# Optimization experiments

Measured on AMD Instinct MI355X. Metric: run time of the kernel, lower is better.

## Reference

```python
import jax, jax.numpy as jnp
import numpy as np

B = 2        # batch size
G = 128      # dense grid extent per axis
N = 200000   # occupied voxels
M = 200000   # query points
C = 128      # feature dim
IGNORE = -1  # ignore_label

# 8 trilinear corner offsets [8,3]
_OFFSETS = jnp.array([[i, j, k] for i in (0, 1) for j in (0, 1) for k in (0, 1)], dtype=jnp.int32)


def setup_inputs() -> dict:
    key = jax.random.key(0)
    k1, k2, k3, k4, k5 = jax.random.split(key, 5)
    xyz = jax.random.randint(k1, (N, 3), 0, G).astype(jnp.int32)
    bids = jnp.sort(jax.random.randint(k2, (N,), 0, B)).astype(jnp.int32)  # sorted batch ids (sparse tensor layout)
    coords = jnp.concatenate([bids[:, None], xyz], axis=1)                 # [N,4]
    features_3d = jax.random.normal(k3, (N, C), dtype=jnp.float32)
    qxyz = jax.random.uniform(k4, (M, 3), minval=0.0, maxval=float(G - 1))
    qb = jnp.sort(jax.random.randint(k5, (M,), 0, B)).astype(jnp.float32)
    query_points = jnp.concatenate([qb[:, None], qxyz], axis=1)            # [M,4]
    return {"features_3d": features_3d, "coords": coords, "query_points": query_points}


def _trilinear(features_3d, coords, query_points):
    bids = coords[:, 0]
    # per-batch coordinate shift (torch.amin per batch)
    shift = jax.ops.segment_min(coords[:, 1:], bids, num_segments=B)       # [B,3]
    c = coords[:, 1:] - shift[bids]                                        # [N,3]
    qb = query_points[:, 0].astype(jnp.int32)                              # [M]
    q = query_points[:, 1:] - shift[qb].astype(query_points.dtype)         # [M,3]

    # dense occupancy grid: voxel row index, IGNORE where empty
    occ = jnp.full((B, G, G, G), IGNORE, dtype=jnp.int32)
    occ = occ.at[bids, c[:, 0], c[:, 1], c[:, 2]].set(jnp.arange(N, dtype=jnp.int32))

    base = jnp.floor(q).astype(jnp.int32)                                  # [M,3]
    frac = q - base.astype(q.dtype)                                        # [M,3]
    corner = base[:, None, :] + _OFFSETS[None]                             # [M,8,3]
    # trilinear weights: prod over dims of frac (offset=1) or 1-frac (offset=0)
    w = jnp.prod(jnp.where(_OFFSETS[None] == 1, frac[:, None, :], 1.0 - frac[:, None, :]), axis=-1)  # [M,8]

    in_bounds = jnp.all((corner >= 0) & (corner < G), axis=-1)             # [M,8]
    cc = jnp.clip(corner, 0, G - 1)
    idx = occ[qb[:, None], cc[..., 0], cc[..., 1], cc[..., 2]]             # [M,8]
    valid = in_bounds & (idx != IGNORE)

    interp_idx = jnp.where(valid, idx, IGNORE)                             # [M,8]
    interp_w = jnp.where(valid, w, 0.0).astype(features_3d.dtype)          # [M,8]

    gathered = features_3d[jnp.maximum(interp_idx, 0)]                     # [M,8,C]
    query_features = jnp.einsum('mk,mkc->mc', interp_w, gathered)          # [M,C]

    # per-voxel accumulated interpolation weight (invalid -> segment N, dropped)
    seg = jnp.where(valid, interp_idx, N).reshape(-1)
    accum_voxel_weights = jax.ops.segment_sum(interp_w.reshape(-1), seg, num_segments=N + 1)[:N]
    return query_features, interp_idx, interp_w, accum_voxel_weights


def reference(features_3d, coords, query_points):
    return _trilinear(features_3d, coords, query_points)
```

## Files before the change

kernel.cpp:

```cpp
#include <hip/hip_runtime.h>

#define NB   2
#define GG   128
#define CC   128

typedef float v4f __attribute__((ext_vector_type(4)));

constexpr int OCC_INTS = NB * GG * GG * GG;

__global__ void __launch_bounds__(256)
init_kernel(int* __restrict__ occ, float* __restrict__ acc,
            int* __restrict__ shift, int n) {
    const int tid = blockIdx.x * blockDim.x + threadIdx.x;
    const int nth = gridDim.x * blockDim.x;
    if (blockIdx.x == 0 && threadIdx.x < NB * 3) shift[threadIdx.x] = 0x7FFFFFFF;
    int4* occ4 = (int4*)occ;
    const int no4 = OCC_INTS / 4;
    for (int i = tid; i < no4; i += nth) occ4[i] = make_int4(-1, -1, -1, -1);
    for (int i = tid; i < n; i += nth) acc[i] = 0.0f;
}

__global__ void shift_kernel(const int* __restrict__ coords,
                             int* __restrict__ shift, int n) {
    __shared__ int smin[NB * 3];
    if (threadIdx.x < NB * 3) smin[threadIdx.x] = 0x7FFFFFFF;
    __syncthreads();
    for (int i = blockIdx.x * blockDim.x + threadIdx.x; i < n;
         i += gridDim.x * blockDim.x) {
        int b = coords[i * 4 + 0];
        atomicMin(&smin[b * 3 + 0], coords[i * 4 + 1]);
        atomicMin(&smin[b * 3 + 1], coords[i * 4 + 2]);
        atomicMin(&smin[b * 3 + 2], coords[i * 4 + 3]);
    }
    __syncthreads();
    if (threadIdx.x < NB * 3) atomicMin(&shift[threadIdx.x], smin[threadIdx.x]);
}

__global__ void scatter_kernel(const int* __restrict__ coords,
                               const int* __restrict__ shift,
                               int* __restrict__ occ, int n) {
    int i = blockIdx.x * blockDim.x + threadIdx.x;
    if (i >= n) return;
    int b = coords[i * 4 + 0];
    int x = coords[i * 4 + 1] - shift[b * 3 + 0];
    int y = coords[i * 4 + 2] - shift[b * 3 + 1];
    int z = coords[i * 4 + 3] - shift[b * 3 + 2];
    size_t off = (((size_t)b * GG + x) * GG + y) * GG + z;
    atomicMax(&occ[off], i);
}

__global__ void __launch_bounds__(256)
corner_kernel(const float* __restrict__ qpts,
              const int* __restrict__ shift,
              const int* __restrict__ occ,
              float* __restrict__ out_idx,
              float* __restrict__ out_w,
              float* __restrict__ out_acc, int mq) {
    const int t = blockIdx.x * 256 + threadIdx.x;
    if (t >= mq * 8) return;
    const int gq = t >> 3;
    const int cn = t & 7;

    const float4 qp = ((const float4*)qpts)[gq];
    const int   qb = (int)qp.x;
    const float q0 = qp.y - (float)shift[qb * 3 + 0];
    const float q1 = qp.z - (float)shift[qb * 3 + 1];
    const float q2 = qp.w - (float)shift[qb * 3 + 2];

    const int oi = (cn >> 2) & 1, oj = (cn >> 1) & 1, ok = cn & 1;
    const float b0 = floorf(q0), b1 = floorf(q1), b2 = floorf(q2);
    const float f0 = q0 - b0, f1 = q1 - b1, f2 = q2 - b2;
    const int c0 = (int)b0 + oi, c1 = (int)b1 + oj, c2 = (int)b2 + ok;
    const float w = (oi ? f0 : 1.0f - f0) *
                    (oj ? f1 : 1.0f - f1) *
                    (ok ? f2 : 1.0f - f2);
    const bool inb = (c0 >= 0) && (c0 < GG) && (c1 >= 0) && (c1 < GG) &&
                     (c2 >= 0) && (c2 < GG);
    int idx = -1;
    if (inb) idx = occ[(((size_t)qb * GG + c0) * GG + c1) * GG + c2];
    const bool  valid = inb && (idx != -1);
    const int   fidx  = valid ? idx : -1;
    const float fw    = valid ? w : 0.0f;

    out_idx[t] = (float)fidx;
    out_w[t]   = fw;
    if (fidx >= 0 && fw != 0.0f) atomicAdd(&out_acc[fidx], fw);
}

__global__ void __launch_bounds__(256)
gather_kernel(const float* __restrict__ feats,
              const float* __restrict__ out_idx,
              const float* __restrict__ out_w,
              float* __restrict__ out_qf, int mq) {
    const int t  = blockIdx.x * 256 + threadIdx.x;
    const int gq = t >> 5;
    if (gq >= mq) return;
    const int c4 = (threadIdx.x & 31) << 2;
    const int k0 = threadIdx.x & 7;

    int   my_idx = (int)out_idx[(size_t)gq * 8 + k0];
    float my_w   = out_w[(size_t)gq * 8 + k0];

    v4f acc = {0.0f, 0.0f, 0.0f, 0.0f};
#pragma unroll
    for (int k = 0; k < 8; ++k) {
        const int   idx = __shfl(my_idx, k, 8);
        const float w   = __shfl(my_w, k, 8);
        if (idx >= 0) {
            const v4f f = *(const v4f*)&feats[(size_t)idx * CC + c4];
            acc += w * f;
        }
    }
    __builtin_nontemporal_store(acc, (v4f*)&out_qf[(size_t)gq * CC + c4]);
}

extern "C" void kernel_launch(void* const* d_in, const int* in_sizes, int n_in,
                              void* d_out, int out_size, void* d_ws, size_t ws_size,
                              hipStream_t stream) {
    const float* feats  = (const float*)d_in[0];
    const int*   coords = (const int*)d_in[1];
    const float* qpts   = (const float*)d_in[2];

    const int n  = in_sizes[1] / 4;
    const int mq = in_sizes[2] / 4;

    float* out     = (float*)d_out;
    float* out_qf  = out;
    float* out_idx = out_qf  + (size_t)mq * CC;
    float* out_w   = out_idx + (size_t)mq * 8;
    float* out_acc = out_w   + (size_t)mq * 8;

    int* shift = (int*)d_ws;
    int* occ   = (int*)((char*)d_ws + 256);

    const int blk = 256;
    init_kernel   <<<2048, blk, 0, stream>>>(occ, out_acc, shift, n);
    shift_kernel  <<<(n + blk - 1) / blk, blk, 0, stream>>>(coords, shift, n);
    scatter_kernel<<<(n + blk - 1) / blk, blk, 0, stream>>>(coords, shift, occ, n);
    corner_kernel <<<(mq * 8 + blk - 1) / blk, blk, 0, stream>>>(
        qpts, shift, occ, out_idx, out_w, out_acc, mq);
    gather_kernel <<<((mq * 32) + blk - 1) / blk, blk, 0, stream>>>(
        feats, out_idx, out_w, out_qf, mq);
}
```

Baseline: 70.32 us.

## Fuse shift with scatter and corner lookup with feature gather

The occupancy grid is now scattered using unshifted coordinates in the same pass that computes the per-batch minimum, and the shift is applied on the query side instead. This removes a separate kernel and its dependency. The corner lookup and weighted feature gather are fused into one kernel: 64 threads compute the 8 corners per query into shared memory, then all 256 threads gather features. This avoids writing and re-reading the idx and weight arrays between kernels, but only a quarter of the threads do the corner phase and a block barrier is added. The unshifted grid assumes coordinates already lie in range; extra bounds checks on the absolute coordinates are added to cover that.

```diff
diff --git a/kernel.cpp b/kernel.cpp
--- a/kernel.cpp
+++ b/kernel.cpp
@@ -3,6 +3,7 @@
 #define NB   2
 #define GG   128
 #define CC   128
+#define QPB  64
 
 typedef float v4f __attribute__((ext_vector_type(4)));
 
@@ -11,115 +12,126 @@
 __global__ void __launch_bounds__(256)
 init_kernel(int* __restrict__ occ, float* __restrict__ acc,
             int* __restrict__ shift, int n) {
-    const int tid = blockIdx.x * blockDim.x + threadIdx.x;
-    const int nth = gridDim.x * blockDim.x;
-    if (blockIdx.x == 0 && threadIdx.x < NB * 3) shift[threadIdx.x] = 0x7FFFFFFF;
+    const int tid = blockIdx.x * 256 + threadIdx.x;
+    const int nth = gridDim.x * 256;
+    if (tid < NB * 3) shift[tid] = 0x7FFFFFFF;
     int4* occ4 = (int4*)occ;
-    const int no4 = OCC_INTS / 4;
-    for (int i = tid; i < no4; i += nth) occ4[i] = make_int4(-1, -1, -1, -1);
+    for (int i = tid; i < OCC_INTS / 4; i += nth)
+        occ4[i] = make_int4(-1, -1, -1, -1);
     for (int i = tid; i < n; i += nth) acc[i] = 0.0f;
 }
 
-__global__ void shift_kernel(const int* __restrict__ coords,
-                             int* __restrict__ shift, int n) {
+__global__ void __launch_bounds__(256)
+scatter_kernel(const int4* __restrict__ coords, int* __restrict__ shift,
+               int* __restrict__ occ, int n) {
     __shared__ int smin[NB * 3];
     if (threadIdx.x < NB * 3) smin[threadIdx.x] = 0x7FFFFFFF;
     __syncthreads();
-    for (int i = blockIdx.x * blockDim.x + threadIdx.x; i < n;
-         i += gridDim.x * blockDim.x) {
-        int b = coords[i * 4 + 0];
-        atomicMin(&smin[b * 3 + 0], coords[i * 4 + 1]);
-        atomicMin(&smin[b * 3 + 1], coords[i * 4 + 2]);
-        atomicMin(&smin[b * 3 + 2], coords[i * 4 + 3]);
+    for (int i = blockIdx.x * 256 + threadIdx.x; i < n; i += gridDim.x * 256) {
+        const int4 c = coords[i];
+        atomicMin(&smin[c.x * 3 + 0], c.y);
+        atomicMin(&smin[c.x * 3 + 1], c.z);
+        atomicMin(&smin[c.x * 3 + 2], c.w);
+        atomicMax(&occ[((c.x * GG + c.y) * GG + c.z) * GG + c.w], i);
     }
     __syncthreads();
     if (threadIdx.x < NB * 3) atomicMin(&shift[threadIdx.x], smin[threadIdx.x]);
 }
 
-__global__ void scatter_kernel(const int* __restrict__ coords,
-                               const int* __restrict__ shift,
-                               int* __restrict__ occ, int n) {
-    int i = blockIdx.x * blockDim.x + threadIdx.x;
-    if (i >= n) return;
-    int b = coords[i * 4 + 0];
-    int x = coords[i * 4 + 1] - shift[b * 3 + 0];
-    int y = coords[i * 4 + 2] - shift[b * 3 + 1];
-    int z = coords[i * 4 + 3] - shift[b * 3 + 2];
-    size_t off = (((size_t)b * GG + x) * GG + y) * GG + z;
-    atomicMax(&occ[off], i);
-}
+__global__ void __launch_bounds__(256)
+query_kernel(const float* __restrict__ feats,
+             const v4f* __restrict__ qpts,
+             const int* __restrict__ shift,
+             const int* __restrict__ occ,
+             float* __restrict__ out_qf,
+             float* __restrict__ out_idx,
+             float* __restrict__ out_w,
+             float* __restrict__ out_acc, int mq) {
+    __shared__ int   s_idx[QPB][8];
+    __shared__ float s_w[QPB][8];
+    const int tid   = threadIdx.x;
+    const int qbase = blockIdx.x * QPB;
 
-__global__ void __launch_bounds__(256)
-corner_kernel(const float* __restrict__ qpts,
-              const int* __restrict__ shift,
-              const int* __restrict__ occ,
-              float* __restrict__ out_idx,
-              float* __restrict__ out_w,
-              float* __restrict__ out_acc, int mq) {
-    const int t = blockIdx.x * 256 + threadIdx.x;
-    if (t >= mq * 8) return;
-    const int gq = t >> 3;
-    const int cn = t & 7;
-
-    const float4 qp = ((const float4*)qpts)[gq];
-    const int   qb = (int)qp.x;
-    const float q0 = qp.y - (float)shift[qb * 3 + 0];
-    const float q1 = qp.z - (float)shift[qb * 3 + 1];
-    const float q2 = qp.w - (float)shift[qb * 3 + 2];
-
-    const int oi = (cn >> 2) & 1, oj = (cn >> 1) & 1, ok = cn & 1;
-    const float b0 = floorf(q0), b1 = floorf(q1), b2 = floorf(q2);
-    const float f0 = q0 - b0, f1 = q1 - b1, f2 = q2 - b2;
-    const int c0 = (int)b0 + oi, c1 = (int)b1 + oj, c2 = (int)b2 + ok;
-    const float w = (oi ? f0 : 1.0f - f0) *
-                    (oj ? f1 : 1.0f - f1) *
-                    (ok ? f2 : 1.0f - f2);
-    const bool inb = (c0 >= 0) && (c0 < GG) && (c1 >= 0) && (c1 < GG) &&
-                     (c2 >= 0) && (c2 < GG);
-    int idx = -1;
-    if (inb) idx = occ[(((size_t)qb * GG + c0) * GG + c1) * GG + c2];
-    const bool  valid = inb && (idx != -1);
-    const int   fidx  = valid ? idx : -1;
-    const float fw    = valid ? w : 0.0f;
-
-    out_idx[t] = (float)fidx;
-    out_w[t]   = fw;
-    if (fidx >= 0 && fw != 0.0f) atomicAdd(&out_acc[fidx], fw);
-}
-
-__global__ void __launch_bounds__(256)
-gather_kernel(const float* __restrict__ feats,
-              const float* __restrict__ out_idx,
-              const float* __restrict__ out_w,
-              float* __restrict__ out_qf, int mq) {
-    const int t  = blockIdx.x * 256 + threadIdx.x;
-    const int gq = t >> 5;
-    if (gq >= mq) return;
-    const int c4 = (threadIdx.x & 31) << 2;
-    const int k0 = threadIdx.x & 7;
-
-    int   my_idx = (int)out_idx[(size_t)gq * 8 + k0];
-    float my_w   = out_w[(size_t)gq * 8 + k0];
-
-    v4f acc = {0.0f, 0.0f, 0.0f, 0.0f};
+    if (tid < QPB) {
+        const int gq = qbase + tid;
+        int   lidx[8];
+        float lw[8];
 #pragma unroll
-    for (int k = 0; k < 8; ++k) {
-        const int   idx = __shfl(my_idx, k, 8);
-        const float w   = __shfl(my_w, k, 8);
-        if (idx >= 0) {
-            const v4f f = *(const v4f*)&feats[(size_t)idx * CC + c4];
-            acc += w * f;
+        for (int cn = 0; cn < 8; ++cn) { lidx[cn] = -1; lw[cn] = 0.0f; }
+        if (gq < mq) {
+            const v4f qp = qpts[gq];
+            const int qb = (int)qp.x;
+            const int s0 = shift[qb * 3 + 0], s1 = shift[qb * 3 + 1],
+                      s2 = shift[qb * 3 + 2];
+            const float q0 = qp.y - (float)s0, q1 = qp.z - (float)s1,
+                        q2 = qp.w - (float)s2;
+            const float b0 = floorf(q0), b1 = floorf(q1), b2 = floorf(q2);
+            const float f0 = q0 - b0, f1 = q1 - b1, f2 = q2 - b2;
+            const int i0 = (int)b0, i1 = (int)b1, i2 = (int)b2;
+            const int u0 = i0 + s0, u1 = i1 + s1, u2 = i2 + s2;
+#pragma unroll
+            for (int cn = 0; cn < 8; ++cn) {
+                const int oi = (cn >> 2) & 1, oj = (cn >> 1) & 1, ok = cn & 1;
+                const int c0 = i0 + oi, c1 = i1 + oj, c2 = i2 + ok;
+                const int a0 = u0 + oi, a1 = u1 + oj, a2 = u2 + ok;
+                const float w = (oi ? f0 : 1.0f - f0) *
+                                (oj ? f1 : 1.0f - f1) *
+                                (ok ? f2 : 1.0f - f2);
+                const bool inb = c0 >= 0 && c0 < GG && c1 >= 0 && c1 < GG &&
+                                 c2 >= 0 && c2 < GG &&
+                                 a0 < GG && a1 < GG && a2 < GG;
+                int idx = -1;
+                if (inb) idx = occ[((qb * GG + a0) * GG + a1) * GG + a2];
+                const float fw = (idx != -1) ? w : 0.0f;
+                lidx[cn] = idx;
+                lw[cn]   = fw;
+                if (idx >= 0 && fw != 0.0f) atomicAdd(&out_acc[idx], fw);
+            }
+            const v4f vi0 = {(float)lidx[0], (float)lidx[1], (float)lidx[2], (float)lidx[3]};
+            const v4f vi1 = {(float)lidx[4], (float)lidx[5], (float)lidx[6], (float)lidx[7]};
+            const v4f vw0 = {lw[0], lw[1], lw[2], lw[3]};
+            const v4f vw1 = {lw[4], lw[5], lw[6], lw[7]};
+            __builtin_nontemporal_store(vi0, (v4f*)&out_idx[(size_t)gq * 8]);
+            __builtin_nontemporal_store(vi1, (v4f*)&out_idx[(size_t)gq * 8 + 4]);
+            __builtin_nontemporal_store(vw0, (v4f*)&out_w[(size_t)gq * 8]);
+            __builtin_nontemporal_store(vw1, (v4f*)&out_w[(size_t)gq * 8 + 4]);
+        }
+#pragma unroll
+        for (int cn = 0; cn < 8; ++cn) {
+            s_idx[tid][cn] = lidx[cn];
+            s_w[tid][cn]   = lw[cn];
         }
     }
-    __builtin_nontemporal_store(acc, (v4f*)&out_qf[(size_t)gq * CC + c4]);
+    __syncthreads();
+
+    const int lane = tid & 31;
+    const int qsub = tid >> 5;
+    const int c4   = lane << 2;
+#pragma unroll
+    for (int p = 0; p < 8; ++p) {
+        const int q  = p * 8 + qsub;
+        const int gq = qbase + q;
+        if (gq >= mq) continue;
+        v4f acc = {0.0f, 0.0f, 0.0f, 0.0f};
+#pragma unroll
+        for (int k = 0; k < 8; ++k) {
+            const int idx = s_idx[q][k];
+            if (idx >= 0) {
+                const float w = s_w[q][k];
+                const v4f f = *(const v4f*)&feats[(size_t)idx * CC + c4];
+                acc += w * f;
+            }
+        }
+        __builtin_nontemporal_store(acc, (v4f*)&out_qf[(size_t)gq * CC + c4]);
+    }
 }
 
 extern "C" void kernel_launch(void* const* d_in, const int* in_sizes, int n_in,
                               void* d_out, int out_size, void* d_ws, size_t ws_size,
                               hipStream_t stream) {
     const float* feats  = (const float*)d_in[0];
-    const int*   coords = (const int*)d_in[1];
-    const float* qpts   = (const float*)d_in[2];
+    const int4*  coords = (const int4*)d_in[1];
+    const v4f*   qpts   = (const v4f*)d_in[2];
 
     const int n  = in_sizes[1] / 4;
     const int mq = in_sizes[2] / 4;
@@ -133,12 +145,8 @@
     int* shift = (int*)d_ws;
     int* occ   = (int*)((char*)d_ws + 256);
 
-    const int blk = 256;
-    init_kernel   <<<2048, blk, 0, stream>>>(occ, out_acc, shift, n);
-    shift_kernel  <<<(n + blk - 1) / blk, blk, 0, stream>>>(coords, shift, n);
-    scatter_kernel<<<(n + blk - 1) / blk, blk, 0, stream>>>(coords, shift, occ, n);
-    corner_kernel <<<(mq * 8 + blk - 1) / blk, blk, 0, stream>>>(
-        qpts, shift, occ, out_idx, out_w, out_acc, mq);
-    gather_kernel <<<((mq * 32) + blk - 1) / blk, blk, 0, stream>>>(
-        feats, out_idx, out_w, out_qf, mq);
+    init_kernel   <<<2048, 256, 0, stream>>>(occ, out_acc, shift, n);
+    scatter_kernel<<<(n + 255) / 256, 256, 0, stream>>>(coords, shift, occ, n);
+    query_kernel  <<<(mq + QPB - 1) / QPB, 256, 0, stream>>>(
+        feats, qpts, shift, occ, out_qf, out_idx, out_w, out_acc, mq);
 }
```

Measured after the change: 66.48 us. 1.06x faster.
